# Performance work log

Measured on AMD Instinct MI355X. Metric: run time of the kernel, lower is better.

## Reference

```python
import jax, jax.numpy as jnp
import numpy as np
import math

D_MODEL = 1024
N_HEADS = 16
N_BINS = 64          # must equal d_head for the original torch broadcast to work
D_LAT = 8
D_HEAD = D_MODEL // N_HEADS


def setup_inputs() -> dict:
    key = jax.random.key(0)
    ks = jax.random.split(key, 12)
    B, S = 4, 4096
    s = 0.02
    return {
        "x": jax.random.normal(ks[0], (B, S, D_MODEL), jnp.float32),
        "Wq": jax.random.normal(ks[1], (D_MODEL, D_MODEL), jnp.float32) * s,
        "bq": jnp.zeros((D_MODEL,), jnp.float32),
        "Wk": jax.random.normal(ks[2], (D_MODEL, D_MODEL), jnp.float32) * s,
        "bk": jnp.zeros((D_MODEL,), jnp.float32),
        "Wv": jax.random.normal(ks[3], (D_MODEL, D_MODEL), jnp.float32) * s,
        "bv": jnp.zeros((D_MODEL,), jnp.float32),
        "Wo": jax.random.normal(ks[4], (D_MODEL, D_MODEL), jnp.float32) * s,
        "bo": jnp.zeros((D_MODEL,), jnp.float32),
        "W_bin": jax.random.normal(ks[5], (D_LAT, D_HEAD), jnp.float32) * s,  # Linear(d_head->d_lat), no bias
        "prototypes": jax.random.normal(ks[6], (N_HEADS, N_BINS, D_LAT), jnp.float32) / math.sqrt(D_LAT),
        "log_tau": jnp.zeros((N_HEADS,), jnp.float32),
    }


def reference(x, Wq, bq, Wk, bk, Wv, bv, Wo, bo, W_bin, prototypes, log_tau):
    B, S, D = x.shape
    H, N, Dh = N_HEADS, N_BINS, D_HEAD

    def proj(W, b):
        return (x @ W.T + b).reshape(B, S, H, Dh).transpose(0, 2, 1, 3)  # [B,H,S,Dh]

    Q = proj(Wq, bq)
    K = proj(Wk, bk)
    V = proj(Wv, bv)

    # bin assignment: project keys to latent, compare to prototypes
    z = jnp.einsum('bhsd,ld->bhsl', K, W_bin)                      # [B,H,S,d_lat]
    tau = jnp.clip(jnp.exp(log_tau), 1e-3)[None, :, None, None]
    logits = jnp.einsum('bhsl,hnl->bhsn', z, prototypes) / (tau + 1e-8)
    logits = logits - jnp.max(logits, axis=-1, keepdims=True)
    attn_probs = jax.nn.softmax(logits.astype(jnp.float32), axis=-1).astype(logits.dtype)  # [B,H,S,N]

    # soft aggregation of K/V into bins
    weighted_K = jnp.einsum('bhsn,bhsd->bhnd', attn_probs, K)      # [B,H,N,Dh]
    weighted_V = jnp.einsum('bhsn,bhsd->bhnd', attn_probs, V)
    counts = jnp.sum(attn_probs, axis=2, keepdims=True)            # [B,H,1,N]
    # NOTE: faithful to the torch code, which broadcasts [B,H,N,Dh]/[B,H,1,N]
    # (valid only because Dh == N): divides feature d by count of bin d.
    K_binned = weighted_K / (counts + 1e-6)
    V_binned = weighted_V / (counts + 1e-6)

    # attention over bins (fp32 scores, matching autocast)
    scores = jnp.einsum('bhsd,bhnd->bhsn', Q.astype(jnp.float32),
                        K_binned.astype(jnp.float32)) / math.sqrt(Dh)
    attn_w = jax.nn.softmax(scores, axis=-1)
    attn_w = jnp.nan_to_num(attn_w, nan=0.0)

    context = jnp.einsum('bhsn,bhnd->bhsd', attn_w.astype(V_binned.dtype), V_binned)
    context = context.transpose(0, 2, 1, 3).reshape(B, S, D)
    return context @ Wo.T + bo
```

## Files before the change

kernel.cpp:

```cpp
#include <hip/hip_runtime.h>
#include <math.h>

typedef float f4 __attribute__((ext_vector_type(4)));
typedef float f32x4 __attribute__((ext_vector_type(4)));
typedef short bf16x8 __attribute__((ext_vector_type(8)));
typedef unsigned int u32x4 __attribute__((ext_vector_type(4)));
typedef unsigned int u32x2 __attribute__((ext_vector_type(2)));
typedef unsigned short u16;
typedef unsigned int u32;

#define D_MODEL 1024
#define N_HEADS 16
#define D_HEAD  64
#define N_BINS  64
#define D_LAT   8

__device__ __forceinline__ unsigned short bf16_rtne(float f) {
    unsigned int u = __builtin_bit_cast(unsigned int, f);
    u += 0x7FFFu + ((u >> 16) & 1u);
    return (unsigned short)(u >> 16);
}
__device__ __forceinline__ float bf16_to_f32(unsigned short h) {
    unsigned int u = ((unsigned int)h) << 16;
    return __builtin_bit_cast(float, u);
}
__device__ __forceinline__ u32 pack_hl(float v) {
    unsigned short h = bf16_rtne(v);
    unsigned short l = bf16_rtne(v - bf16_to_f32(h));
    return (u32)h | ((u32)l << 16);
}
__device__ __forceinline__ void unpack8(const u32* p, bf16x8& hf, bf16x8& lf) {
    u32x4 r0 = *(const u32x4*)p;
    u32x4 r1 = *(const u32x4*)(p + 4);
    u32x4 hv, lv;
    hv[0] = (r0[0] & 0xffffu) | (r0[1] << 16);  lv[0] = (r0[0] >> 16) | (r0[1] & 0xffff0000u);
    hv[1] = (r0[2] & 0xffffu) | (r0[3] << 16);  lv[1] = (r0[2] >> 16) | (r0[3] & 0xffff0000u);
    hv[2] = (r1[0] & 0xffffu) | (r1[1] << 16);  lv[2] = (r1[0] >> 16) | (r1[1] & 0xffff0000u);
    hv[3] = (r1[2] & 0xffffu) | (r1[3] << 16);  lv[3] = (r1[2] >> 16) | (r1[3] & 0xffff0000u);
    hf = __builtin_bit_cast(bf16x8, hv);
    lf = __builtin_bit_cast(bf16x8, lv);
}

__global__ __launch_bounds__(256)
void split_bf16x2(const float* __restrict__ in, unsigned short* __restrict__ hi,
                  unsigned short* __restrict__ lo, int n8)
{
    int i = blockIdx.x * 256 + threadIdx.x;
    if (i >= n8) return;
    const f4* inp = (const f4*)in;
    f4 a = inp[2 * i];
    f4 b = inp[2 * i + 1];
    unsigned short hs[8], ls[8];
#pragma unroll
    for (int j = 0; j < 8; j++) {
        float v = (j < 4) ? a[j] : b[j - 4];
        unsigned short h = bf16_rtne(v);
        hs[j] = h;
        ls[j] = bf16_rtne(v - bf16_to_f32(h));
    }
    u32x4 ho, lv;
#pragma unroll
    for (int j = 0; j < 4; j++) {
        ho[j] = (unsigned int)hs[2 * j] | ((unsigned int)hs[2 * j + 1] << 16);
        lv[j] = (unsigned int)ls[2 * j] | ((unsigned int)ls[2 * j + 1] << 16);
    }
    ((u32x4*)hi)[i] = ho;
    ((u32x4*)lo)[i] = lv;
}

__global__ __launch_bounds__(256)
void split4_w(const float* __restrict__ w0, const float* __restrict__ w1,
              const float* __restrict__ w2, const float* __restrict__ w3,
              unsigned short* __restrict__ hi, unsigned short* __restrict__ lo)
{
    const int which = blockIdx.y;
    const float* in = (which == 0) ? w0 : (which == 1) ? w1 : (which == 2) ? w2 : w3;
    int i = blockIdx.x * 256 + threadIdx.x;
    const f4* inp = (const f4*)in;
    f4 a = inp[2 * i];
    f4 b = inp[2 * i + 1];
    unsigned short hs[8], ls[8];
#pragma unroll
    for (int j = 0; j < 8; j++) {
        float v = (j < 4) ? a[j] : b[j - 4];
        unsigned short h = bf16_rtne(v);
        hs[j] = h;
        ls[j] = bf16_rtne(v - bf16_to_f32(h));
    }
    u32x4 ho, lv;
#pragma unroll
    for (int j = 0; j < 4; j++) {
        ho[j] = (unsigned int)hs[2 * j] | ((unsigned int)hs[2 * j + 1] << 16);
        lv[j] = (unsigned int)ls[2 * j] | ((unsigned int)ls[2 * j + 1] << 16);
    }
    size_t off = (size_t)which * (D_MODEL * D_MODEL / 8);
    ((u32x4*)hi)[off + i] = ho;
    ((u32x4*)lo)[off + i] = lv;
}

__device__ __forceinline__ void glds16(const unsigned short* g, unsigned short* l) {
    __builtin_amdgcn_global_load_lds((const __attribute__((address_space(1))) void*)g,
                                     (__attribute__((address_space(3))) void*)l,
                                     16, 0, 0);
}

template<bool SPLIT>
__global__ __launch_bounds__(512)
void gemm_bf16x2_nt(const unsigned short* __restrict__ Ahi, const unsigned short* __restrict__ Alo,
                    const unsigned short* __restrict__ Bhi, const unsigned short* __restrict__ Blo,
                    const float* __restrict__ bias, float* __restrict__ C,
                    unsigned short* __restrict__ Chi, unsigned short* __restrict__ Clo,
                    int M, int N, int K)
{
    __shared__ unsigned short lds[2][4][8192];

    const int tid  = threadIdx.x;
    const int lane = tid & 63;
    const int w    = tid >> 6;
    const int wm   = w >> 2;
    const int wn   = w & 3;
    const int bm   = blockIdx.x * 256;
    const int bn   = blockIdx.y * 256;

    const int schunk = (lane & 3) ^ ((lane >> 3) & 3);
    size_t gA[2], gB[2];
    int    seg[2];
#pragma unroll
    for (int i = 0; i < 2; i++) {
        int s = i * 8 + w;
        int r = s * 16 + (lane >> 2);
        gA[i]  = (size_t)(bm + r) * K + schunk * 8;
        gB[i]  = (size_t)(bn + r) * K + schunk * 8;
        seg[i] = s * 512;
    }

    const int koff  = ((lane >> 4) ^ ((lane >> 1) & 3)) * 8;
    const int abase = (wm * 128 + (lane & 15)) * 32 + koff;
    const int bbase = (wn * 64  + (lane & 15)) * 32 + koff;

    f32x4 acc[8][4];
#pragma unroll
    for (int i = 0; i < 8; i++)
#pragma unroll
        for (int j = 0; j < 4; j++) acc[i][j] = (f32x4){0.f, 0.f, 0.f, 0.f};

    auto stage = [&](int bb, int kt) {
#pragma unroll
        for (int i = 0; i < 2; i++) {
            glds16(Ahi + gA[i] + kt, &lds[bb][0][seg[i]]);
            glds16(Alo + gA[i] + kt, &lds[bb][1][seg[i]]);
            glds16(Bhi + gB[i] + kt, &lds[bb][2][seg[i]]);
            glds16(Blo + gB[i] + kt, &lds[bb][3][seg[i]]);
        }
    };

    stage(0, 0);
    __syncthreads();

    const int nt = K / 32;
    for (int t = 0; t < nt; t++) {
        const int cur = t & 1;
        if (t + 1 < nt) stage(cur ^ 1, (t + 1) * 32);

        bf16x8 bhf[4], blf[4];
#pragma unroll
        for (int fn = 0; fn < 4; fn++) {
            bhf[fn] = *(const bf16x8*)&lds[cur][2][bbase + fn * 512];
            blf[fn] = *(const bf16x8*)&lds[cur][3][bbase + fn * 512];
        }
#pragma unroll
        for (int half = 0; half < 2; half++) {
            bf16x8 ahf[4], alf[4];
#pragma unroll
            for (int i = 0; i < 4; i++) {
                ahf[i] = *(const bf16x8*)&lds[cur][0][abase + (half * 4 + i) * 512];
                alf[i] = *(const bf16x8*)&lds[cur][1][abase + (half * 4 + i) * 512];
            }
#pragma unroll
            for (int i = 0; i < 4; i++)
#pragma unroll
                for (int fn = 0; fn < 4; fn++) {
                    f32x4 a = acc[half * 4 + i][fn];
                    a = __builtin_amdgcn_mfma_f32_16x16x32_bf16(ahf[i], bhf[fn], a, 0, 0, 0);
                    a = __builtin_amdgcn_mfma_f32_16x16x32_bf16(ahf[i], blf[fn], a, 0, 0, 0);
                    a = __builtin_amdgcn_mfma_f32_16x16x32_bf16(alf[i], bhf[fn], a, 0, 0, 0);
                    acc[half * 4 + i][fn] = a;
                }
        }
        __syncthreads();
    }

    const int rb = bm + wm * 128;
    const int cb = bn + wn * 64;
    float bv[4];
#pragma unroll
    for (int fn = 0; fn < 4; fn++) bv[fn] = bias[cb + fn * 16 + (lane & 15)];
#pragma unroll
    for (int fm = 0; fm < 8; fm++)
#pragma unroll
        for (int e = 0; e < 4; e++) {
            size_t row = (size_t)(rb + fm * 16 + (lane >> 4) * 4 + e);
            if constexpr (SPLIT) {
#pragma unroll
                for (int fn = 0; fn < 4; fn++) {
                    float v = acc[fm][fn][e] + bv[fn];
                    unsigned short h = bf16_rtne(v);
                    Chi[row * N + cb + fn * 16 + (lane & 15)] = h;
                    Clo[row * N + cb + fn * 16 + (lane & 15)] = bf16_rtne(v - bf16_to_f32(h));
                }
            } else {
                float* cp = &C[row * N];
#pragma unroll
                for (int fn = 0; fn < 4; fn++)
                    cp[cb + fn * 16 + (lane & 15)] = acc[fm][fn][e] + bv[fn];
            }
        }
}

__global__ __launch_bounds__(256)
void bin_assign_agg(const float* __restrict__ Kbuf, const float* __restrict__ Vbuf,
                    const float* __restrict__ W_bin, const float* __restrict__ proto,
                    const float* __restrict__ log_tau,
                    float* __restrict__ partials, int B, int S)
{
    __shared__ __attribute__((aligned(16))) float Wb[8][64];
    __shared__ __attribute__((aligned(16))) float Prt[8][64];
    __shared__ __attribute__((aligned(16))) float zsm[64][8];
    __shared__ __attribute__((aligned(16))) float Kt[64][68];
    __shared__ __attribute__((aligned(16))) u32 KT32[64][68];
    __shared__ __attribute__((aligned(16))) u32 VT32[64][68];
    __shared__ __attribute__((aligned(16))) u32 P32T[64][68];

    const int bh = blockIdx.x;
    const int h  = bh & (N_HEADS - 1);
    const int b  = bh >> 4;
    const int chunk = blockIdx.y;
    const int CH = gridDim.y;
    const int tid = threadIdx.x;
    const int lane = tid & 63;
    const int w = tid >> 6;

    if (tid < 128) {
        ((f4*)&Wb[0][0])[tid] = ((const f4*)W_bin)[tid];
    } else {
        int t = tid - 128;
        f4 p = ((const f4*)(proto + (size_t)h * N_BINS * D_LAT))[t];
        int n = t >> 1, l4 = (t & 1) * 4;
        Prt[l4 + 0][n] = p[0];
        Prt[l4 + 1][n] = p[1];
        Prt[l4 + 2][n] = p[2];
        Prt[l4 + 3][n] = p[3];
    }
    const float tau   = fmaxf(expf(log_tau[h]), 1e-3f);
    const float scale = 1.0f / (tau + 1e-8f);

    const int row = tid >> 2, sub = tid & 3;
    const int lr = lane & 15, lc = lane >> 4;
    const int mat = w >> 1;
    const int fn0 = (w & 1) * 2;

    f32x4 acc[4][2];
    f4 cntv[4];
#pragma unroll
    for (int i = 0; i < 4; i++) {
        cntv[i] = (f4){0.f, 0.f, 0.f, 0.f};
        acc[i][0] = (f32x4){0.f, 0.f, 0.f, 0.f};
        acc[i][1] = (f32x4){0.f, 0.f, 0.f, 0.f};
    }

    const int SC = S / CH;
    const int s_base = chunk * SC;

    for (int s0 = 0; s0 < SC; s0 += 64) {
        __syncthreads();
#pragma unroll
        for (int q = 0; q < 2; q++) {
            int item = tid + 256 * q;
            int rp = item >> 4;
            int dc = item & 15;
            int r0 = rp * 2;
            size_t gi = ((size_t)(b * S + s_base + s0 + r0)) * D_MODEL + h * D_HEAD + dc * 4;
            f4 k0 = *(const f4*)&Kbuf[gi];
            f4 k1 = *(const f4*)&Kbuf[gi + D_MODEL];
            f4 v0 = *(const f4*)&Vbuf[gi];
            f4 v1 = *(const f4*)&Vbuf[gi + D_MODEL];
            *(f4*)&Kt[r0][dc * 4]     = k0;
            *(f4*)&Kt[r0 + 1][dc * 4] = k1;
#pragma unroll
            for (int j = 0; j < 4; j++) {
                int d = dc * 4 + j;
                *(u32x2*)&KT32[d][r0] = (u32x2){pack_hl(k0[j]), pack_hl(k1[j])};
                *(u32x2*)&VT32[d][r0] = (u32x2){pack_hl(v0[j]), pack_hl(v1[j])};
            }
        }
        __syncthreads();

        {
            const int l0 = sub * 2;
            f4 z0 = {0.f, 0.f, 0.f, 0.f}, z1 = {0.f, 0.f, 0.f, 0.f};
#pragma unroll
            for (int d4 = 0; d4 < 16; d4++) {
                f4 kv = *(const f4*)&Kt[row][d4 * 4];
                f4 w0 = *(const f4*)&Wb[l0][d4 * 4];
                f4 w1 = *(const f4*)&Wb[l0 + 1][d4 * 4];
                z0 += kv * w0;
                z1 += kv * w1;
            }
            zsm[row][l0]     = z0[0] + z0[1] + z0[2] + z0[3];
            zsm[row][l0 + 1] = z1[0] + z1[1] + z1[2] + z1[3];
        }
        __syncthreads();

        {
            float zr[8];
#pragma unroll
            for (int l = 0; l < 8; l++) zr[l] = zsm[row][l];
            f4 lg[4];
#pragma unroll
            for (int q = 0; q < 4; q++) lg[q] = (f4){0.f, 0.f, 0.f, 0.f};
#pragma unroll
            for (int l = 0; l < 8; l++) {
                float zv = zr[l];
#pragma unroll
                for (int q = 0; q < 4; q++) {
                    f4 pr = *(const f4*)&Prt[l][sub * 16 + q * 4];
                    lg[q] += zv * pr;
                }
            }
            float mx = -1e30f;
#pragma unroll
            for (int q = 0; q < 4; q++) {
                lg[q] *= scale;
                mx = fmaxf(mx, fmaxf(fmaxf(lg[q][0], lg[q][1]), fmaxf(lg[q][2], lg[q][3])));
            }
            mx = fmaxf(mx, __shfl_xor(mx, 1));
            mx = fmaxf(mx, __shfl_xor(mx, 2));
            float sum = 0.f;
            f4 pv[4];
#pragma unroll
            for (int q = 0; q < 4; q++) {
#pragma unroll
                for (int e = 0; e < 4; e++) {
                    float ev = expf(lg[q][e] - mx);
                    pv[q][e] = ev;
                    sum += ev;
                }
            }
            sum += __shfl_xor(sum, 1);
            sum += __shfl_xor(sum, 2);
            float inv = 1.0f / sum;
#pragma unroll
            for (int q = 0; q < 4; q++) {
                pv[q] *= inv;
                cntv[q] += pv[q];
#pragma unroll
                for (int e = 0; e < 4; e++)
                    P32T[sub * 16 + q * 4 + e][row] = pack_hl(pv[q][e]);
            }
        }
        __syncthreads();

#pragma unroll
        for (int ks = 0; ks < 2; ks++) {
            bf16x8 pah[4], pal[4];
#pragma unroll
            for (int fm = 0; fm < 4; fm++)
                unpack8(&P32T[fm * 16 + lr][ks * 32 + lc * 8], pah[fm], pal[fm]);
#pragma unroll
            for (int fnL = 0; fnL < 2; fnL++) {
                int dr = (fn0 + fnL) * 16 + lr;
                bf16x8 bhf, blf;
                const u32* bp = mat ? &VT32[dr][ks * 32 + lc * 8]
                                    : &KT32[dr][ks * 32 + lc * 8];
                unpack8(bp, bhf, blf);
#pragma unroll
                for (int fm = 0; fm < 4; fm++) {
                    f32x4 a = acc[fm][fnL];
                    a = __builtin_amdgcn_mfma_f32_16x16x32_bf16(pah[fm], bhf, a, 0, 0, 0);
                    a = __builtin_amdgcn_mfma_f32_16x16x32_bf16(pah[fm], blf, a, 0, 0, 0);
                    a = __builtin_amdgcn_mfma_f32_16x16x32_bf16(pal[fm], bhf, a, 0, 0, 0);
                    acc[fm][fnL] = a;
                }
            }
        }
    }

#pragma unroll
    for (int q = 0; q < 4; q++)
#pragma unroll
        for (int e = 0; e < 4; e++) {
            float c = cntv[q][e];
            c += __shfl_xor(c, 4);
            c += __shfl_xor(c, 8);
            c += __shfl_xor(c, 16);
            c += __shfl_xor(c, 32);
            cntv[q][e] = c;
        }

    float* base = partials + ((size_t)bh * CH + chunk) * 8448;
#pragma unroll
    for (int fm = 0; fm < 4; fm++)
#pragma unroll
        for (int fnL = 0; fnL < 2; fnL++)
#pragma unroll
            for (int e = 0; e < 4; e++) {
                int n = fm * 16 + lc * 4 + e;
                int d = (fn0 + fnL) * 16 + lr;
                base[mat * 4096 + (size_t)n * 64 + d] = acc[fm][fnL][e];
            }
    if ((lane >> 2) == 0) {
#pragma unroll
        for (int q = 0; q < 4; q++)
#pragma unroll
            for (int e = 0; e < 4; e++)
                base[8192 + w * 64 + sub * 16 + q * 4 + e] = cntv[q][e];
    }
}

__global__ __launch_bounds__(256)
void bin_reduce(const float* __restrict__ partials,
                u16* __restrict__ Kbh, u16* __restrict__ Kbl,
                u16* __restrict__ Vth, u16* __restrict__ Vtl, int CH)
{
    const int bh = blockIdx.x;
    const int tid = threadIdx.x;
    __shared__ float inv_cnt[64];
    const float* base = partials + (size_t)bh * CH * 8448;
    if (tid < 64) {
        float c = 0.f;
        for (int ch = 0; ch < CH; ch++)
#pragma unroll
            for (int ww = 0; ww < 4; ww++)
                c += base[(size_t)ch * 8448 + 8192 + ww * 64 + tid];
        inv_cnt[tid] = 1.0f / (c + 1e-6f);
    }
    __syncthreads();
    for (int idx = tid; idx < 4096; idx += 256) {
        float k = 0.f, v = 0.f;
        for (int ch = 0; ch < CH; ch++) {
            const float* p = base + (size_t)ch * 8448;
            k += p[idx];
            v += p[4096 + idx];
        }
        float ic = inv_cnt[idx & 63];
        k *= ic;
        v *= ic;
        int n = idx >> 6, d = idx & 63;
        u16 kh = bf16_rtne(k);
        Kbh[(size_t)bh * 4096 + idx] = kh;
        Kbl[(size_t)bh * 4096 + idx] = bf16_rtne(k - bf16_to_f32(kh));
        u16 vh = bf16_rtne(v);
        size_t ti = (size_t)bh * 4096 + (size_t)d * 64 + n;
        Vth[ti] = vh;
        Vtl[ti] = bf16_rtne(v - bf16_to_f32(vh));
    }
}

__global__ __launch_bounds__(256)
void bin_attn_mfma(const u16* __restrict__ Qhi, const u16* __restrict__ Qlo,
                   const u16* __restrict__ Kbh, const u16* __restrict__ Kbl,
                   const u16* __restrict__ Vth, const u16* __restrict__ Vtl,
                   u16* __restrict__ ctx_hi, u16* __restrict__ ctx_lo,
                   int B, int S)
{
    __shared__ unsigned int P32[4][64][68];

    const int bh = blockIdx.x;
    const int h  = bh & (N_HEADS - 1);
    const int b  = bh >> 4;
    const int tid = threadIdx.x;
    const int l  = tid & 63;
    const int w  = tid >> 6;
    const int s0 = blockIdx.y * 256 + w * 64;

    const int lr = l & 15;
    const int lc = l >> 4;

    const size_t qoff  = ((size_t)(b * S + s0 + lr)) * D_MODEL + h * D_HEAD + lc * 8;
    const size_t kboff = (size_t)bh * 4096 + (size_t)lr * 64 + lc * 8;

    f32x4 acc[4][4];
#pragma unroll
    for (int i = 0; i < 4; i++)
#pragma unroll
        for (int j = 0; j < 4; j++) acc[i][j] = (f32x4){0.f, 0.f, 0.f, 0.f};

#pragma unroll
    for (int ks = 0; ks < 2; ks++) {
        bf16x8 qh[4], ql[4], kh[4], kl[4];
#pragma unroll
        for (int f = 0; f < 4; f++) {
            qh[f] = *(const bf16x8*)(Qhi + qoff + f * 16 * D_MODEL + ks * 32);
            ql[f] = *(const bf16x8*)(Qlo + qoff + f * 16 * D_MODEL + ks * 32);
            kh[f] = *(const bf16x8*)(Kbh + kboff + f * 1024 + ks * 32);
            kl[f] = *(const bf16x8*)(Kbl + kboff + f * 1024 + ks * 32);
        }
#pragma unroll
        for (int fm = 0; fm < 4; fm++)
#pragma unroll
            for (int fn = 0; fn < 4; fn++) {
                acc[fm][fn] = __builtin_amdgcn_mfma_f32_16x16x32_bf16(qh[fm], kh[fn], acc[fm][fn], 0, 0, 0);
                acc[fm][fn] = __builtin_amdgcn_mfma_f32_16x16x32_bf16(qh[fm], kl[fn], acc[fm][fn], 0, 0, 0);
                acc[fm][fn] = __builtin_amdgcn_mfma_f32_16x16x32_bf16(ql[fm], kh[fn], acc[fm][fn], 0, 0, 0);
            }
    }

#pragma unroll
    for (int fm = 0; fm < 4; fm++) {
#pragma unroll
        for (int e = 0; e < 4; e++) {
            float v0 = acc[fm][0][e] * 0.125f;
            float v1 = acc[fm][1][e] * 0.125f;
            float v2 = acc[fm][2][e] * 0.125f;
            float v3 = acc[fm][3][e] * 0.125f;
            float mx = fmaxf(fmaxf(v0, v1), fmaxf(v2, v3));
            mx = fmaxf(mx, __shfl_xor(mx, 1));
            mx = fmaxf(mx, __shfl_xor(mx, 2));
            mx = fmaxf(mx, __shfl_xor(mx, 4));
            mx = fmaxf(mx, __shfl_xor(mx, 8));
            float e0 = expf(v0 - mx), e1 = expf(v1 - mx);
            float e2 = expf(v2 - mx), e3 = expf(v3 - mx);
            float sum = e0 + e1 + e2 + e3;
            sum += __shfl_xor(sum, 1);
            sum += __shfl_xor(sum, 2);
            sum += __shfl_xor(sum, 4);
            sum += __shfl_xor(sum, 8);
            float inv = 1.0f / sum;
            float pv[4] = {e0 * inv, e1 * inv, e2 * inv, e3 * inv};
            int rowi = fm * 16 + lc * 4 + e;
#pragma unroll
            for (int fn = 0; fn < 4; fn++)
                P32[w][rowi][fn * 16 + lr] = pack_hl(pv[fn]);
        }
    }

    f32x4 acc2[4][4];
#pragma unroll
    for (int i = 0; i < 4; i++)
#pragma unroll
        for (int j = 0; j < 4; j++) acc2[i][j] = (f32x4){0.f, 0.f, 0.f, 0.f};

#pragma unroll
    for (int ks = 0; ks < 2; ks++) {
        bf16x8 vh[4], vl[4];
#pragma unroll
        for (int f = 0; f < 4; f++) {
            vh[f] = *(const bf16x8*)(Vth + kboff + f * 1024 + ks * 32);
            vl[f] = *(const bf16x8*)(Vtl + kboff + f * 1024 + ks * 32);
        }
        bf16x8 ph[4], pl[4];
#pragma unroll
        for (int fm = 0; fm < 4; fm++)
            unpack8(&P32[w][fm * 16 + lr][ks * 32 + lc * 8], ph[fm], pl[fm]);
#pragma unroll
        for (int fm = 0; fm < 4; fm++)
#pragma unroll
            for (int fn = 0; fn < 4; fn++) {
                acc2[fm][fn] = __builtin_amdgcn_mfma_f32_16x16x32_bf16(ph[fm], vh[fn], acc2[fm][fn], 0, 0, 0);
                acc2[fm][fn] = __builtin_amdgcn_mfma_f32_16x16x32_bf16(ph[fm], vl[fn], acc2[fm][fn], 0, 0, 0);
                acc2[fm][fn] = __builtin_amdgcn_mfma_f32_16x16x32_bf16(pl[fm], vh[fn], acc2[fm][fn], 0, 0, 0);
            }
    }

    const size_t gbase = ((size_t)(b * S + s0 + lc * 4)) * D_MODEL + h * D_HEAD + lr;
#pragma unroll
    for (int fm = 0; fm < 4; fm++)
#pragma unroll
        for (int e = 0; e < 4; e++) {
            size_t ro = gbase + ((size_t)(fm * 16 + e)) * D_MODEL;
#pragma unroll
            for (int fn = 0; fn < 4; fn++) {
                float v = acc2[fm][fn][e];
                u16 hv = bf16_rtne(v);
                ctx_hi[ro + fn * 16] = hv;
                ctx_lo[ro + fn * 16] = bf16_rtne(v - bf16_to_f32(hv));
            }
        }
}

extern "C" void kernel_launch(void* const* d_in, const int* in_sizes, int n_in,
                              void* d_out, int out_size, void* d_ws, size_t ws_size,
                              hipStream_t stream)
{
    (void)n_in; (void)out_size; (void)ws_size;
    const float* x       = (const float*)d_in[0];
    const float* Wq      = (const float*)d_in[1];
    const float* bq      = (const float*)d_in[2];
    const float* Wk      = (const float*)d_in[3];
    const float* bk      = (const float*)d_in[4];
    const float* Wv      = (const float*)d_in[5];
    const float* bv      = (const float*)d_in[6];
    const float* Wo      = (const float*)d_in[7];
    const float* bo      = (const float*)d_in[8];
    const float* W_bin   = (const float*)d_in[9];
    const float* proto   = (const float*)d_in[10];
    const float* log_tau = (const float*)d_in[11];
    float* out = (float*)d_out;

    const int M  = in_sizes[0] / D_MODEL;
    const int S  = 4096;
    const int B  = M / S;
    const int BH = B * N_HEADS;
    const int CH = 8;

    const size_t MB = (size_t)1 << 20;
    char* wsb = (char*)d_ws;
    float*          R1   = (float*)wsb;
    float*          R2   = (float*)(wsb + 64  * MB);
    unsigned short* XShi = (unsigned short*)(wsb + 128 * MB);
    unsigned short* XSlo = (unsigned short*)(wsb + 160 * MB);
    unsigned short* W4hi = (unsigned short*)(wsb + 192 * MB);
    unsigned short* W4lo = (unsigned short*)(wsb + 200 * MB);
    u16*            Kbh  = (u16*)(wsb + 208 * MB);
    u16*            Kbl  = Kbh + (size_t)BH * 4096;
    u16*            Vth  = Kbl + (size_t)BH * 4096;
    u16*            Vtl  = Vth + (size_t)BH * 4096;

    float* part = (float*)d_out;

    u16* Qhi = (u16*)R1;
    u16* Qlo = Qhi + (size_t)M * D_MODEL;

    const size_t WOFF = (size_t)D_MODEL * D_MODEL;
    const int n8x = (M * D_MODEL) / 8;
    const int n8w = (D_MODEL * D_MODEL) / 8;
    dim3 gg(M / 256, D_MODEL / 256);

    split_bf16x2<<<n8x / 256, 256, 0, stream>>>(x, XShi, XSlo, n8x);
    split4_w<<<dim3(n8w / 256, 4), 256, 0, stream>>>(Wq, Wk, Wv, Wo, W4hi, W4lo);

    gemm_bf16x2_nt<false><<<gg, 512, 0, stream>>>(XShi, XSlo, W4hi + WOFF, W4lo + WOFF,
                                                  bk, R1, nullptr, nullptr,
                                                  M, D_MODEL, D_MODEL);
    gemm_bf16x2_nt<false><<<gg, 512, 0, stream>>>(XShi, XSlo, W4hi + 2 * WOFF, W4lo + 2 * WOFF,
                                                  bv, R2, nullptr, nullptr,
                                                  M, D_MODEL, D_MODEL);

    bin_assign_agg<<<dim3(BH, CH), 256, 0, stream>>>(R1, R2, W_bin, proto,
                                                     log_tau, part, B, S);
    bin_reduce<<<BH, 256, 0, stream>>>(part, Kbh, Kbl, Vth, Vtl, CH);

    gemm_bf16x2_nt<true><<<gg, 512, 0, stream>>>(XShi, XSlo, W4hi, W4lo,
                                                 bq, nullptr, Qhi, Qlo,
                                                 M, D_MODEL, D_MODEL);

    bin_attn_mfma<<<dim3(BH, S / 256), 256, 0, stream>>>(Qhi, Qlo, Kbh, Kbl, Vth, Vtl,
                                                         XShi, XSlo, B, S);

    gemm_bf16x2_nt<false><<<gg, 512, 0, stream>>>(XShi, XSlo, W4hi + 3 * WOFF, W4lo + 3 * WOFF,
                                                  bo, out, nullptr, nullptr,
                                                  M, D_MODEL, D_MODEL);
}
```

Before: 499.7 us.

## Interleave GEMM global-to-LDS prefetch with MFMA quadrants using explicit barriers and priority

```diff
diff --git a/kernel.cpp b/kernel.cpp
--- a/kernel.cpp
+++ b/kernel.cpp
@@ -104,6 +104,14 @@
                                      16, 0, 0);
 }
 
+#define MFMA3(ACC, AH, AL, BH, BL) do {                                        \
+    f32x4 _a = (ACC);                                                          \
+    _a = __builtin_amdgcn_mfma_f32_16x16x32_bf16((AH), (BH), _a, 0, 0, 0);     \
+    _a = __builtin_amdgcn_mfma_f32_16x16x32_bf16((AH), (BL), _a, 0, 0, 0);     \
+    _a = __builtin_amdgcn_mfma_f32_16x16x32_bf16((AL), (BH), _a, 0, 0, 0);     \
+    (ACC) = _a;                                                                \
+} while (0)
+
 template<bool SPLIT>
 __global__ __launch_bounds__(512)
 void gemm_bf16x2_nt(const unsigned short* __restrict__ Ahi, const unsigned short* __restrict__ Alo,
@@ -144,50 +152,98 @@
 #pragma unroll
         for (int j = 0; j < 4; j++) acc[i][j] = (f32x4){0.f, 0.f, 0.f, 0.f};
 
-    auto stage = [&](int bb, int kt) {
-#pragma unroll
-        for (int i = 0; i < 2; i++) {
-            glds16(Ahi + gA[i] + kt, &lds[bb][0][seg[i]]);
-            glds16(Alo + gA[i] + kt, &lds[bb][1][seg[i]]);
-            glds16(Bhi + gB[i] + kt, &lds[bb][2][seg[i]]);
-            glds16(Blo + gB[i] + kt, &lds[bb][3][seg[i]]);
-        }
-    };
-
-    stage(0, 0);
-    __syncthreads();
+#pragma unroll
+    for (int i = 0; i < 2; i++) {
+        glds16(Ahi + gA[i], &lds[0][0][seg[i]]);
+        glds16(Alo + gA[i], &lds[0][1][seg[i]]);
+        glds16(Bhi + gB[i], &lds[0][2][seg[i]]);
+        glds16(Blo + gB[i], &lds[0][3][seg[i]]);
+    }
+    asm volatile("s_waitcnt vmcnt(0)" ::: "memory");
+    __builtin_amdgcn_s_barrier();
 
     const int nt = K / 32;
     for (int t = 0; t < nt; t++) {
         const int cur = t & 1;
-        if (t + 1 < nt) stage(cur ^ 1, (t + 1) * 32);
-
-        bf16x8 bhf[4], blf[4];
-#pragma unroll
-        for (int fn = 0; fn < 4; fn++) {
-            bhf[fn] = *(const bf16x8*)&lds[cur][2][bbase + fn * 512];
-            blf[fn] = *(const bf16x8*)&lds[cur][3][bbase + fn * 512];
-        }
-#pragma unroll
-        for (int half = 0; half < 2; half++) {
-            bf16x8 ahf[4], alf[4];
-#pragma unroll
-            for (int i = 0; i < 4; i++) {
-                ahf[i] = *(const bf16x8*)&lds[cur][0][abase + (half * 4 + i) * 512];
-                alf[i] = *(const bf16x8*)&lds[cur][1][abase + (half * 4 + i) * 512];
-            }
-#pragma unroll
-            for (int i = 0; i < 4; i++)
-#pragma unroll
-                for (int fn = 0; fn < 4; fn++) {
-                    f32x4 a = acc[half * 4 + i][fn];
-                    a = __builtin_amdgcn_mfma_f32_16x16x32_bf16(ahf[i], bhf[fn], a, 0, 0, 0);
-                    a = __builtin_amdgcn_mfma_f32_16x16x32_bf16(ahf[i], blf[fn], a, 0, 0, 0);
-                    a = __builtin_amdgcn_mfma_f32_16x16x32_bf16(alf[i], bhf[fn], a, 0, 0, 0);
-                    acc[half * 4 + i][fn] = a;
-                }
-        }
-        __syncthreads();
+        const int nxt = cur ^ 1;
+        const bool pre = (t + 1 < nt);
+        const int kt = (t + 1) * 32;
+
+        bf16x8 a0h[4], a0l[4], a1h[4], a1l[4];
+        bf16x8 b0h[2], b0l[2], b1h[2], b1l[2];
+
+#pragma unroll
+        for (int i = 0; i < 4; i++) {
+            a0h[i] = *(const bf16x8*)&lds[cur][0][abase + i * 512];
+            a0l[i] = *(const bf16x8*)&lds[cur][1][abase + i * 512];
+        }
+#pragma unroll
+        for (int j = 0; j < 2; j++) {
+            b0h[j] = *(const bf16x8*)&lds[cur][2][bbase + j * 512];
+            b0l[j] = *(const bf16x8*)&lds[cur][3][bbase + j * 512];
+        }
+        if (pre) {
+            glds16(Ahi + gA[0] + kt, &lds[nxt][0][seg[0]]);
+            glds16(Ahi + gA[1] + kt, &lds[nxt][0][seg[1]]);
+        }
+        __builtin_amdgcn_s_setprio(1);
+#pragma unroll
+        for (int i = 0; i < 4; i++)
+#pragma unroll
+            for (int j = 0; j < 2; j++)
+                MFMA3(acc[i][j], a0h[i], a0l[i], b0h[j], b0l[j]);
+        __builtin_amdgcn_s_setprio(0);
+        __builtin_amdgcn_s_barrier();
+
+#pragma unroll
+        for (int j = 0; j < 2; j++) {
+            b1h[j] = *(const bf16x8*)&lds[cur][2][bbase + (2 + j) * 512];
+            b1l[j] = *(const bf16x8*)&lds[cur][3][bbase + (2 + j) * 512];
+        }
+        if (pre) {
+            glds16(Alo + gA[0] + kt, &lds[nxt][1][seg[0]]);
+            glds16(Alo + gA[1] + kt, &lds[nxt][1][seg[1]]);
+        }
+        __builtin_amdgcn_s_setprio(1);
+#pragma unroll
+        for (int i = 0; i < 4; i++)
+#pragma unroll
+            for (int j = 0; j < 2; j++)
+                MFMA3(acc[i][2 + j], a0h[i], a0l[i], b1h[j], b1l[j]);
+        __builtin_amdgcn_s_setprio(0);
+        __builtin_amdgcn_s_barrier();
+
+#pragma unroll
+        for (int i = 0; i < 4; i++) {
+            a1h[i] = *(const bf16x8*)&lds[cur][0][abase + (4 + i) * 512];
+            a1l[i] = *(const bf16x8*)&lds[cur][1][abase + (4 + i) * 512];
+        }
+        if (pre) {
+            glds16(Bhi + gB[0] + kt, &lds[nxt][2][seg[0]]);
+            glds16(Bhi + gB[1] + kt, &lds[nxt][2][seg[1]]);
+        }
+        __builtin_amdgcn_s_setprio(1);
+#pragma unroll
+        for (int i = 0; i < 4; i++)
+#pragma unroll
+            for (int j = 0; j < 2; j++)
+                MFMA3(acc[4 + i][j], a1h[i], a1l[i], b0h[j], b0l[j]);
+        __builtin_amdgcn_s_setprio(0);
+        __builtin_amdgcn_s_barrier();
+
+        if (pre) {
+            glds16(Blo + gB[0] + kt, &lds[nxt][3][seg[0]]);
+            glds16(Blo + gB[1] + kt, &lds[nxt][3][seg[1]]);
+        }
+        __builtin_amdgcn_s_setprio(1);
+#pragma unroll
+        for (int i = 0; i < 4; i++)
+#pragma unroll
+            for (int j = 0; j < 2; j++)
+                MFMA3(acc[4 + i][2 + j], a1h[i], a1l[i], b1h[j], b1l[j]);
+        __builtin_amdgcn_s_setprio(0);
+        asm volatile("s_waitcnt vmcnt(0)" ::: "memory");
+        __builtin_amdgcn_s_barrier();
     }
 
     const int rb = bm + wm * 128;
@@ -601,7 +657,7 @@
     const int S  = 4096;
     const int B  = M / S;
     const int BH = B * N_HEADS;
-    const int CH = 8;
+    const int CH = 16;
 
     const size_t MB = (size_t)1 << 20;
     char* wsb = (char*)d_ws;
```

After: 540.4 us. 1.08x slower.
